# Performance work log

Hardware: AMD Instinct MI355X
Metric: run time of the kernel (lower is better)

The kernel has to match this reference:

```python
import jax, jax.numpy as jnp
import numpy as np

DIM = 512
MAX_STEP = 4
SLOTS = 8


def _lin(x, w, b):
    # torch nn.Linear convention: w is [out, in]
    return jnp.matmul(x, jnp.swapaxes(w, -1, -2)) + b


def setup_inputs() -> dict:
    B, L, HW, d, S, K = 512, 32, 196, DIM, MAX_STEP, SLOTS
    ks = iter(jax.random.split(jax.random.key(0), 48))
    def rn(shape, scale=1.0):
        return scale * jax.random.normal(next(ks), shape, dtype=jnp.float32)
    p = 0.05  # weight init scale
    z = lambda *s: jnp.zeros(s, jnp.float32)
    return {
        'context': rn((B, L, d)),
        'question': rn((B, 2 * d)),
        'knowledge': rn((B, d, HW)),
        'kb_proj': rn((B, d, HW)),
        'control': rn((B, d)),
        'memory': rn((B, d)),
        'history': rn((B, d, K)),
        'Wt_sequential': jnp.zeros((B, 1, K), jnp.float32).at[:, :, 0].set(1.0),
        # ControlUnit params (per-step position-aware linears, control-question linear, attention linear)
        'ctrl_pos_w': rn((S, d, 2 * d), p), 'ctrl_pos_b': z(S, d),
        'ctrl_cq_w': rn((d, 2 * d), p), 'ctrl_cq_b': z(d),
        'ctrl_attn_w': rn((1, d), p), 'ctrl_attn_b': z(1),
        # ReadUnit params (memory proj, concat proj, attention)
        'read_mem_w': rn((d, d), p), 'read_mem_b': z(d),
        'read_cat_w': rn((d, 2 * d), p), 'read_cat_b': z(d),
        'read_attn_w': rn((1, d), p), 'read_attn_b': z(1),
        # ReadMemory params (same structure, over the slot history)
        'rm_mem_w': rn((d, d), p), 'rm_mem_b': z(d),
        'rm_cat_w': rn((d, 2 * d), p), 'rm_cat_b': z(d),
        'rm_attn_w': rn((1, d), p), 'rm_attn_b': z(1),
        # WriteUnit (no self-attention / no memory gate)
        'write_w': rn((d, 2 * d), p), 'write_b': z(d),
        # linear_read gate MLP (2d -> 2d -> 1)
        'lr_w1': rn((2 * d, 2 * d), p), 'lr_b1': z(2 * d),
        'lr_w2': rn((1, 2 * d), p), 'lr_b2': z(1),
        # linear_read_history gate MLP
        'lrh_w1': rn((2 * d, 2 * d), p), 'lrh_b1': z(2 * d),
        'lrh_w2': rn((1, 2 * d), p), 'lrh_b2': z(1),
        # linear_layer_mix_context MLP (d -> d -> 3)
        'mix_w1': rn((d, d), p), 'mix_b1': z(d),
        'mix_w2': rn((3, d), p), 'mix_b2': z(3),
    }


def _forward(context, question, knowledge, kb_proj, control, memory, history, Wt_sequential,
             ctrl_pos_w, ctrl_pos_b, ctrl_cq_w, ctrl_cq_b, ctrl_attn_w, ctrl_attn_b,
             read_mem_w, read_mem_b, read_cat_w, read_cat_b, read_attn_w, read_attn_b,
             rm_mem_w, rm_mem_b, rm_cat_w, rm_cat_b, rm_attn_w, rm_attn_b,
             write_w, write_b, lr_w1, lr_b1, lr_w2, lr_b2,
             lrh_w1, lrh_b1, lrh_w2, lrh_b2, mix_w1, mix_b1, mix_w2, mix_b2):
    K = history.shape[2]
    # shift-by-one circulant matrix, matches the hard-coded convolution_kernel for slots in {4,6,8}
    conv_kernel = jnp.roll(jnp.eye(K, dtype=history.dtype), -1, axis=1)
    for i in range(MAX_STEP):
        # --- ControlUnit: attention over contextual words ---
        pa = _lin(question, ctrl_pos_w[i], ctrl_pos_b[i])                                  # [B,d]
        cqi = _lin(jnp.concatenate([control, pa], axis=1), ctrl_cq_w, ctrl_cq_b)           # [B,d]
        cvi = jax.nn.softmax(_lin(cqi[:, None, :] * context, ctrl_attn_w, ctrl_attn_b), axis=1)  # [B,L,1]
        control = jnp.sum(cvi * context, axis=1)                                           # [B,d]
        # --- ReadUnit: attention over the knowledge base ---
        mem_p = _lin(memory, read_mem_w, read_mem_b)[:, :, None]                           # [B,d,1]
        cat = jnp.concatenate([mem_p * kb_proj, kb_proj], axis=1)                          # [B,2d,HW]
        feat = _lin(cat.transpose(0, 2, 1), read_cat_w, read_cat_b)                        # [B,HW,d]
        attn = jax.nn.softmax(_lin(feat * control[:, None, :], read_attn_w, read_attn_b), axis=1)
        attn = attn.transpose(0, 2, 1)                                                     # [B,1,HW]
        read = jnp.sum(attn * knowledge, axis=2)                                           # [B,d]
        # --- ReadMemory: attention over the slot history ---
        memh = _lin(memory, rm_mem_w, rm_mem_b)[:, :, None]                                # [B,d,1]
        cath = jnp.concatenate([memh * history, history], axis=1)                          # [B,2d,K]
        feath = _lin(cath.transpose(0, 2, 1), rm_cat_w, rm_cat_b)                          # [B,K,d]
        rvi_h = jax.nn.softmax(_lin(feath * control[:, None, :], rm_attn_w, rm_attn_b), axis=1).transpose(0, 2, 1)  # [B,1,K]
        read_h = jnp.sum(rvi_h * history, axis=2)                                          # [B,d]
        # --- gates ---
        gkb = jax.nn.sigmoid(_lin(jax.nn.elu(_lin(jnp.concatenate([control, read], axis=1), lr_w1, lr_b1)), lr_w2, lr_b2))      # [B,1]
        gmem = jax.nn.sigmoid(_lin(jax.nn.elu(_lin(jnp.concatenate([control, read_h], axis=1), lrh_w1, lrh_b1)), lrh_w2, lrh_b2))  # [B,1]
        # --- gated addressable memory write (NTM-style) ---
        wts = Wt_sequential[:, 0, :]                                                       # [B,K]
        W = (gmem * rvi_h[:, 0, :] + wts * (1.0 - gmem)) * gkb                             # [B,K]
        history = history * (1.0 - W[:, None, :]) + read[:, :, None] * W[:, None, :]       # erase + add
        first = (1.0 - gmem) * gkb                                                         # [B,1]
        Wt_sequential = ((wts @ conv_kernel) * first + wts * (1.0 - first))[:, None, :]    # [B,1,K]
        # --- context mixing + write ---
        now_ctx = gkb * read
        last_ctx = gmem * read_h
        latest_ctx = (1.0 - gkb) * last_ctx + now_ctx
        cwv = jax.nn.softmax(_lin(jax.nn.elu(_lin(control, mix_w1, mix_b1)), mix_w2, mix_b2), axis=1)  # [B,3]
        ctx_read = cwv[:, 0:1] * now_ctx + cwv[:, 1:2] * last_ctx + cwv[:, 2:3] * latest_ctx
        memory = _lin(jnp.concatenate([ctx_read, memory], axis=1), write_w, write_b)       # [B,d]
    return memory


reference = _forward
```

## Files before the change

kernel.cpp:

```cpp
#include <hip/hip_runtime.h>
#include <cstddef>

constexpr int NB   = 512;
constexpr int ND   = 512;
constexpr int NL   = 32;
constexpr int NHW  = 196;
constexpr int NK   = 8;
constexpr int NSTEP = 4;

typedef __attribute__((ext_vector_type(8))) short short8v;
typedef __attribute__((ext_vector_type(4))) float f32x4;

__device__ __forceinline__ void splitbf(float x, short& h, short& l) {
    unsigned u  = __float_as_uint(x);
    unsigned hb = (u + 0x7FFFu + ((u >> 16) & 1u)) & 0xFFFF0000u;
    h = (short)(hb >> 16);
    float rem = x - __uint_as_float(hb);
    unsigned v = __float_as_uint(rem);
    l = (short)((v + 0x7FFFu + ((v >> 16) & 1u)) >> 16);
}
__device__ __forceinline__ unsigned short f2bf(float x) {
    unsigned u = __float_as_uint(x);
    return (unsigned short)((u + 0x7FFFu + ((u >> 16) & 1u)) >> 16);
}
__device__ __forceinline__ float bf2f(unsigned short h) {
    return __uint_as_float(((unsigned)h) << 16);
}

struct GP {
    const short *A1h, *A1l, *A2h, *A2l;
    const short *Bh, *Bl;
    const float* bias;
    float* C; short* Ch; short* Cl;
    int lda1, lda2, k1, N, K, ntN, tile0;
};
struct GPG { GP p[3]; int np; };

template<int ACT>
__global__ __launch_bounds__(256) void ggemm_k(GPG g)
{
    __shared__ short Ah[32][40], Al[32][40], Bh_s[64][40], Bl_s[64][40];
    const int flat = blockIdx.x;
    int pi = 0;
    if (g.np > 1 && flat >= g.p[1].tile0) pi = 1;
    if (g.np > 2 && flat >= g.p[2].tile0) pi = 2;
    const GP p = g.p[pi];
    const int local = flat - p.tile0;
    const int my = local / p.ntN, nx = local - my * p.ntN;
    const int m0 = my * 32, n0 = nx * 64;
    const int t = threadIdx.x, lane = t & 63, wid = t >> 6;
    const int wr = wid >> 1, wc = wid & 1;
    const int lr = lane & 15, lk = (lane >> 4) * 8;
    const int ar = (t & 127) >> 2, ak = (t & 3) * 8;
    const bool alo = t >= 128;
    const int br = t >> 2, bk = (t & 3) * 8;

    f32x4 acc0 = {}, acc1 = {};
    for (int kt = 0; kt < p.K; kt += 32) {
        {
            const int gk = kt + ak;
            const short* srcp = (gk < p.k1)
                ? (alo ? p.A1l : p.A1h) + (size_t)(m0 + ar) * p.lda1 + gk
                : (alo ? p.A2l : p.A2h) + (size_t)(m0 + ar) * p.lda2 + (gk - p.k1);
            short8v v = *(const short8v*)srcp;
            if (alo) *(short8v*)&Al[ar][ak] = v;
            else     *(short8v*)&Ah[ar][ak] = v;
        }
        {
            const size_t off = (size_t)(n0 + br) * p.K + kt + bk;
            *(short8v*)&Bh_s[br][bk] = *(const short8v*)(p.Bh + off);
            *(short8v*)&Bl_s[br][bk] = *(const short8v*)(p.Bl + off);
        }
        __syncthreads();
        short8v ah  = *(short8v*)&Ah[wr * 16 + lr][lk];
        short8v al  = *(short8v*)&Al[wr * 16 + lr][lk];
        short8v bh0 = *(short8v*)&Bh_s[wc * 32      + lr][lk];
        short8v bh1 = *(short8v*)&Bh_s[wc * 32 + 16 + lr][lk];
        short8v bl0 = *(short8v*)&Bl_s[wc * 32      + lr][lk];
        short8v bl1 = *(short8v*)&Bl_s[wc * 32 + 16 + lr][lk];
        acc0 = __builtin_amdgcn_mfma_f32_16x16x32_bf16(ah, bh0, acc0, 0, 0, 0);
        acc1 = __builtin_amdgcn_mfma_f32_16x16x32_bf16(ah, bh1, acc1, 0, 0, 0);
        acc0 = __builtin_amdgcn_mfma_f32_16x16x32_bf16(al, bh0, acc0, 0, 0, 0);
        acc1 = __builtin_amdgcn_mfma_f32_16x16x32_bf16(al, bh1, acc1, 0, 0, 0);
        acc0 = __builtin_amdgcn_mfma_f32_16x16x32_bf16(ah, bl0, acc0, 0, 0, 0);
        acc1 = __builtin_amdgcn_mfma_f32_16x16x32_bf16(ah, bl1, acc1, 0, 0, 0);
        __syncthreads();
    }
    const int r0 = m0 + wr * 16 + ((lane >> 4) << 2);
    const int cb = n0 + wc * 32 + lr;
    #pragma unroll
    for (int fc = 0; fc < 2; ++fc) {
        const f32x4& a = fc ? acc1 : acc0;
        const int col = cb + fc * 16;
        const float badd = p.bias ? p.bias[col] : 0.f;
        #pragma unroll
        for (int rr = 0; rr < 4; ++rr) {
            float x = a[rr] + badd;
            if (ACT == 1) x = (x > 0.f) ? x : (expf(x) - 1.f);
            const size_t idx = (size_t)(r0 + rr) * p.N + col;
            if (p.C) p.C[idx] = x;
            if (p.Ch) { short h, l; splitbf(x, h, l); p.Ch[idx] = h; p.Cl[idx] = l; }
        }
    }
}

struct WSeg { const float* src; short* dh; short* dl; int n; };
struct WTab { WSeg s[12]; int total; };

__global__ __launch_bounds__(256) void wconv_k(WTab tab)
{
    int i = blockIdx.x * 256 + threadIdx.x;
    if (i >= tab.total) return;
    int seg = 0, off = i;
    while (off >= tab.s[seg].n) { off -= tab.s[seg].n; ++seg; }
    short h, l; splitbf(tab.s[seg].src[off], h, l);
    tab.s[seg].dh[off] = h;
    tab.s[seg].dl[off] = l;
}

__global__ __launch_bounds__(256) void tconv_k(
    const float* s0, short* dh0, short* dl0,
    const float* s1, short* dh1, short* dl1)
{
    const float* src = blockIdx.z ? s1 : s0;
    short* dh = blockIdx.z ? dh1 : dh0;
    short* dl = blockIdx.z ? dl1 : dl0;
    __shared__ float tile[32][33];
    const int n0 = blockIdx.x * 32, k0 = blockIdx.y * 32;
    const int tx = threadIdx.x & 31, ty = threadIdx.x >> 5;
    for (int i = ty; i < 32; i += 8)
        tile[i][tx] = src[(size_t)(k0 + i) * 1024 + n0 + tx];
    __syncthreads();
    for (int i = ty; i < 32; i += 8) {
        short h, l; splitbf(tile[tx][i], h, l);
        dh[(size_t)(n0 + i) * 512 + k0 + tx] = h;
        dl[(size_t)(n0 + i) * 512 + k0 + tx] = l;
    }
}

__global__ __launch_bounds__(512) void ctrl_attn_k(
    const float* __restrict__ cqi, const float* __restrict__ context,
    const float* __restrict__ attn_w, const float* __restrict__ read_attn_w,
    const float* __restrict__ rm_attn_w,
    short* __restrict__ ct_h, short* __restrict__ ct_l,
    short* __restrict__ cw_h, short* __restrict__ cw_l,
    short* __restrict__ cx_h, short* __restrict__ cx_l)
{
    const int b = blockIdx.x, t = threadIdx.x;
    const int lane = t & 63, w = t >> 6;
    __shared__ float q[ND];
    __shared__ float p[NL];
    const float* ctx = context + (size_t)b * NL * ND;

    q[t] = cqi[(size_t)b * ND + t] * attn_w[t];
    __syncthreads();

    for (int l = w; l < NL; l += 8) {
        float s = 0.f;
        const float* row = ctx + (size_t)l * ND;
        #pragma unroll
        for (int d = lane; d < ND; d += 64) s += q[d] * row[d];
        #pragma unroll
        for (int o = 32; o; o >>= 1) s += __shfl_down(s, o);
        if (lane == 0) p[l] = s;
    }
    __syncthreads();
    if (t == 0) {
        float mx = p[0];
        for (int l = 1; l < NL; ++l) mx = fmaxf(mx, p[l]);
        float sum = 0.f;
        for (int l = 0; l < NL; ++l) { float e = expf(p[l] - mx); p[l] = e; sum += e; }
        const float inv = 1.f / sum;
        for (int l = 0; l < NL; ++l) p[l] *= inv;
    }
    __syncthreads();
    float a = 0.f;
    #pragma unroll 8
    for (int l = 0; l < NL; ++l) a += p[l] * ctx[(size_t)l * ND + t];
    const size_t ix = (size_t)b * ND + t;
    short h, l2;
    splitbf(a, h, l2);                     ct_h[ix] = h; ct_l[ix] = l2;
    splitbf(a * read_attn_w[t], h, l2);    cw_h[ix] = h; cw_l[ix] = l2;
    splitbf(a * rm_attn_w[t],  h, l2);     cx_h[ix] = h; cx_l[ix] = l2;
}

template<int FIRST>
__global__ __launch_bounds__(256) void kbsh_k(
    const float* __restrict__ kbp_f32, unsigned short* __restrict__ kbp_bf,
    const float* __restrict__ mpc, const float* __restrict__ u,
    float* __restrict__ s_part,
    const float* __restrict__ hist, const float* __restrict__ uh,
    float* __restrict__ rvi, float* __restrict__ read_h,
    short* __restrict__ rh_h, short* __restrict__ rh_l)
{
    __shared__ float sh[NK * ND + ND];
    __shared__ float sred[NK], pk[NK];
    const int bx = blockIdx.x, t = threadIdx.x;
    const int lane = t & 63, w = t >> 6;

    if (bx < 4 * NB) {
        const int jc = bx >> 9, b = bx & 511;
        float* v = sh;
        const int j0 = jc * 128;
        if (t < 128) {
            const int j = j0 + t;
            v[t] = mpc[(size_t)b * 1024 + j] * u[(size_t)b * 1024 + j]
                 + u[(size_t)b * 1024 + 512 + j];
        }
        __syncthreads();
        if (t < NHW) {
            const size_t base = (size_t)b * ND * NHW + (size_t)j0 * NHW + t;
            float s = 0.f;
            #pragma unroll 4
            for (int j = 0; j < 128; ++j) {
                float x;
                if (FIRST) {
                    x = kbp_f32[base + (size_t)j * NHW];
                    kbp_bf[base + (size_t)j * NHW] = f2bf(x);
                } else {
                    x = bf2f(kbp_bf[base + (size_t)j * NHW]);
                }
                s += x * v[j];
            }
            s_part[((size_t)jc * NB + b) * 200 + t] = s;
        }
    } else {
        const int b = bx - 4 * NB;
        float* ht = sh;
        float* vh = sh + NK * ND;
        const float* hb = hist + (size_t)b * ND * NK;

        for (int dd = t; dd < ND; dd += 256) {
            float4 h0 = *(const float4*)&hb[(size_t)dd * NK];
            float4 h1 = *(const float4*)&hb[(size_t)dd * NK + 4];
            ht[0 * ND + dd] = h0.x; ht[1 * ND + dd] = h0.y;
            ht[2 * ND + dd] = h0.z; ht[3 * ND + dd] = h0.w;
            ht[4 * ND + dd] = h1.x; ht[5 * ND + dd] = h1.y;
            ht[6 * ND + dd] = h1.z; ht[7 * ND + dd] = h1.w;
            vh[dd] = mpc[(size_t)b * 1024 + 512 + dd] * uh[(size_t)b * 1024 + dd]
                   + uh[(size_t)b * 1024 + 512 + dd];
        }
        __syncthreads();

        for (int k = w; k < NK; k += 4) {
            float s = 0.f;
            #pragma unroll 4
            for (int dd = lane; dd < ND; dd += 64) s += ht[k * ND + dd] * vh[dd];
            #pragma unroll
            for (int o = 32; o; o >>= 1) s += __shfl_down(s, o);
            if (lane == 0) sred[k] = s;
        }
        __syncthreads();
        if (t == 0) {
            float mx = sred[0];
            #pragma unroll
            for (int k = 1; k < NK; ++k) mx = fmaxf(mx, sred[k]);
            float ev[NK]; float sum = 0.f;
            #pragma unroll
            for (int k = 0; k < NK; ++k) { ev[k] = expf(sred[k] - mx); sum += ev[k]; }
            const float inv = 1.f / sum;
            #pragma unroll
            for (int k = 0; k < NK; ++k) { float pv = ev[k] * inv; pk[k] = pv; rvi[(size_t)b * NK + k] = pv; }
        }
        __syncthreads();
        for (int dd = t; dd < ND; dd += 256) {
            float a = 0.f;
// ... 166 lines not shown
{
    (void)in_sizes; (void)n_in; (void)out_size; (void)ws_size;
    const float* context    = (const float*)d_in[0];
    const float* question   = (const float*)d_in[1];
    const float* knowledge  = (const float*)d_in[2];
    const float* kb_proj    = (const float*)d_in[3];
    const float* control0   = (const float*)d_in[4];
    const float* memory0    = (const float*)d_in[5];
    const float* history0   = (const float*)d_in[6];
    const float* wt0        = (const float*)d_in[7];
    const float* ctrl_pos_w = (const float*)d_in[8];
    const float* ctrl_pos_b = (const float*)d_in[9];
    const float* ctrl_cq_w  = (const float*)d_in[10];
    const float* ctrl_cq_b  = (const float*)d_in[11];
    const float* ctrl_attn_w= (const float*)d_in[12];
    const float* read_mem_w = (const float*)d_in[14];
    const float* read_mem_b = (const float*)d_in[15];
    const float* read_cat_w = (const float*)d_in[16];
    const float* read_attn_w= (const float*)d_in[18];
    const float* rm_mem_w   = (const float*)d_in[20];
    const float* rm_mem_b   = (const float*)d_in[21];
    const float* rm_cat_w   = (const float*)d_in[22];
    const float* rm_attn_w  = (const float*)d_in[24];
    const float* write_w    = (const float*)d_in[26];
    const float* write_b    = (const float*)d_in[27];
    const float* lr_w1      = (const float*)d_in[28];
    const float* lr_b1      = (const float*)d_in[29];
    const float* lr_w2      = (const float*)d_in[30];
    const float* lr_b2      = (const float*)d_in[31];
    const float* lrh_w1     = (const float*)d_in[32];
    const float* lrh_b1     = (const float*)d_in[33];
    const float* lrh_w2     = (const float*)d_in[34];
    const float* lrh_b2     = (const float*)d_in[35];
    const float* mix_w1     = (const float*)d_in[36];
    const float* mix_b1     = (const float*)d_in[37];
    const float* mix_w2     = (const float*)d_in[38];
    const float* mix_b2     = (const float*)d_in[39];

    float* f = (float*)d_ws;
    auto takef = [&](size_t n) { float* p = f; f += n; return p; };
    float* cqi    = takef((size_t)NB * ND);
    float* mpc    = takef((size_t)NB * 1024);
    float* u      = takef((size_t)NB * 1024);
    float* uh     = takef((size_t)NB * 1024);
    float* readv  = takef((size_t)NB * ND);
    float* read_h = takef((size_t)NB * ND);
    float* rvi    = takef((size_t)NB * NK);
    float* g1a    = takef((size_t)NB * 1024);
    float* g1b    = takef((size_t)NB * 1024);
    float* m1buf  = takef((size_t)NB * ND);
    float* hist   = takef((size_t)NB * ND * NK);
    float* wts    = takef((size_t)NB * NK);
    float* s_part = takef((size_t)4 * NB * 200);
    float* bcat   = takef(1024);

    uintptr_t fa = ((uintptr_t)f + 15) & ~(uintptr_t)15;
    short* s = (short*)fa;
    auto takes = [&](size_t n) { short* p = s; s += n; return p; };
    short* cpw_h = takes((size_t)2048 * 1024); short* cpw_l = takes((size_t)2048 * 1024);
    short* cqw_h = takes((size_t)512 * 1024);  short* cqw_l = takes((size_t)512 * 1024);
    short* wmc_h = takes((size_t)1024 * 512);  short* wmc_l = takes((size_t)1024 * 512);
    short* rcw_h = takes((size_t)1024 * 512);  short* rcw_l = takes((size_t)1024 * 512);
    short* rmw_h = takes((size_t)1024 * 512);  short* rmw_l = takes((size_t)1024 * 512);
    short* lrw_h = takes((size_t)1024 * 1024); short* lrw_l = takes((size_t)1024 * 1024);
    short* lhw_h = takes((size_t)1024 * 1024); short* lhw_l = takes((size_t)1024 * 1024);
    short* mxw_h = takes((size_t)512 * 512);   short* mxw_l = takes((size_t)512 * 512);
    short* ww_h  = takes((size_t)512 * 1024);  short* ww_l  = takes((size_t)512 * 1024);
    short* q_h   = takes((size_t)512 * 1024);  short* q_l   = takes((size_t)512 * 1024);
    short* c0_h  = takes((size_t)NB * ND);     short* c0_l  = takes((size_t)NB * ND);
    short* m0_h  = takes((size_t)NB * ND);     short* m0_l  = takes((size_t)NB * ND);
    short* pa_h  = takes((size_t)NB * 2048);   short* pa_l  = takes((size_t)NB * 2048);
    short* ct_h  = takes((size_t)NB * ND);     short* ct_l  = takes((size_t)NB * ND);
    short* cw_h  = takes((size_t)NB * ND);     short* cw_l  = takes((size_t)NB * ND);
    short* cwh_h = takes((size_t)NB * ND);     short* cwh_l = takes((size_t)NB * ND);
    short* rv_h  = takes((size_t)NB * ND);     short* rv_l  = takes((size_t)NB * ND);
    short* rh_h  = takes((size_t)NB * ND);     short* rh_l  = takes((size_t)NB * ND);
    short* cx_h  = takes((size_t)NB * ND);     short* cx_l  = takes((size_t)NB * ND);
    short* mA_h  = takes((size_t)NB * ND);     short* mA_l  = takes((size_t)NB * ND);
    short* mB_h  = takes((size_t)NB * ND);     short* mB_l  = takes((size_t)NB * ND);
    short* mC_h  = takes((size_t)NB * ND);     short* mC_l  = takes((size_t)NB * ND);
    unsigned short* kbp_bf = (unsigned short*)s;
    unsigned short* knw_bf = kbp_bf + (size_t)NB * ND * NHW;

    hipMemcpyAsync(hist, history0, sizeof(float) * NB * ND * NK, hipMemcpyDeviceToDevice, stream);
    hipMemcpyAsync(wts,  wt0,      sizeof(float) * NB * NK,      hipMemcpyDeviceToDevice, stream);
    hipMemcpyAsync(bcat,       read_mem_b, sizeof(float) * 512, hipMemcpyDeviceToDevice, stream);
    hipMemcpyAsync(bcat + 512, rm_mem_b,   sizeof(float) * 512, hipMemcpyDeviceToDevice, stream);

    WTab tab;
    tab.s[0]  = {ctrl_pos_w, cpw_h, cpw_l, 2048 * 1024};
    tab.s[1]  = {ctrl_cq_w,  cqw_h, cqw_l, 512 * 1024};
    tab.s[2]  = {read_mem_w, wmc_h, wmc_l, 512 * 512};
    tab.s[3]  = {rm_mem_w,   wmc_h + 512 * 512, wmc_l + 512 * 512, 512 * 512};
    tab.s[4]  = {lr_w1,  lrw_h, lrw_l, 1024 * 1024};
    tab.s[5]  = {lrh_w1, lhw_h, lhw_l, 1024 * 1024};
    tab.s[6]  = {mix_w1, mxw_h, mxw_l, 512 * 512};
    tab.s[7]  = {write_w, ww_h, ww_l, 512 * 1024};
    tab.s[8]  = {question, q_h, q_l, 512 * 1024};
    tab.s[9]  = {control0, c0_h, c0_l, 512 * 512};
    tab.s[10] = {memory0,  m0_h, m0_l, 512 * 512};
    tab.s[11] = {nullptr, nullptr, nullptr, 0};
    tab.total = 2048*1024 + 512*1024 + 512*512 + 512*512 + 1024*1024 + 1024*1024
              + 512*512 + 512*1024 + 512*1024 + 512*512 + 512*512;
    wconv_k<<<dim3((tab.total + 255) / 256), dim3(256), 0, stream>>>(tab);
    tconv_k<<<dim3(32, 16, 2), dim3(256), 0, stream>>>(read_cat_w, rcw_h, rcw_l,
                                                       rm_cat_w,  rmw_h, rmw_l);

    auto P = [](const short* A1h, const short* A1l, int lda1, int k1,
                const short* A2h, const short* A2l, int lda2,
                const short* Bh, const short* Bl, const float* bias,
                float* C, short* Ch, short* Cl, int N, int K, int tile0) {
        GP q; q.A1h = A1h; q.A1l = A1l; q.A2h = A2h; q.A2l = A2l;
        q.Bh = Bh; q.Bl = Bl; q.bias = bias; q.C = C; q.Ch = Ch; q.Cl = Cl;
        q.lda1 = lda1; q.lda2 = lda2; q.k1 = k1; q.N = N; q.K = K;
        q.ntN = N / 64; q.tile0 = tile0;
        return q;
    };
    auto tilesOf = [](int N) { return (NB / 32) * (N / 64); };
    auto GG = [&](GPG g, int total, int act) {
        if (act) ggemm_k<1><<<dim3(total), dim3(256), 0, stream>>>(g);
        else     ggemm_k<0><<<dim3(total), dim3(256), 0, stream>>>(g);
    };

    {
        GPG g; g.np = 1;
        g.p[0] = P(q_h, q_l, 1024, 1024, q_h, q_l, 1024, cpw_h, cpw_l, ctrl_pos_b,
                   nullptr, pa_h, pa_l, 2048, 1024, 0);
        GG(g, tilesOf(2048), 0);
    }

    const short* mems_h[4] = {m0_h, mA_h, mB_h, mC_h};
    const short* mems_l[4] = {m0_l, mA_l, mB_l, mC_l};
    const short* ctl_h = c0_h;
    const short* ctl_l = c0_l;

    for (int i = 0; i < NSTEP; ++i) {
        {
            GPG g; int nt = 0, np = 0;
            if (i > 0) {
                g.p[np++] = P(cx_h, cx_l, ND, ND, mems_h[i - 1], mems_l[i - 1], ND,
                              ww_h, ww_l, write_b, nullptr,
                              (short*)mems_h[i], (short*)mems_l[i], ND, 1024, nt);
                nt += tilesOf(ND);
            }
            g.p[np++] = P(ctl_h, ctl_l, ND, ND, pa_h + (size_t)i * ND, pa_l + (size_t)i * ND, 2048,
                          cqw_h, cqw_l, ctrl_cq_b, cqi, nullptr, nullptr, ND, 1024, nt);
            nt += tilesOf(ND);
            g.np = np;
            GG(g, nt, 0);
        }
        ctrl_attn_k<<<dim3(NB), dim3(512), 0, stream>>>(cqi, context, ctrl_attn_w,
                                                        read_attn_w, rm_attn_w,
                                                        ct_h, ct_l, cw_h, cw_l, cwh_h, cwh_l);
        ctl_h = ct_h; ctl_l = ct_l;
        {
            GPG g; g.np = 3;
            g.p[0] = P(mems_h[i], mems_l[i], ND, ND, mems_h[i], mems_l[i], ND,
                       wmc_h, wmc_l, bcat, mpc, nullptr, nullptr, 1024, 512, 0);
            g.p[1] = P(cw_h, cw_l, ND, ND, cw_h, cw_l, ND,
                       rcw_h, rcw_l, nullptr, u, nullptr, nullptr, 1024, 512, 256);
            g.p[2] = P(cwh_h, cwh_l, ND, ND, cwh_h, cwh_l, ND,
                       rmw_h, rmw_l, nullptr, uh, nullptr, nullptr, 1024, 512, 512);
            GG(g, 768, 0);
        }
        if (i == 0)
            kbsh_k<1><<<dim3(5 * NB), dim3(256), 0, stream>>>(kb_proj, kbp_bf, mpc, u, s_part,
                                                              hist, uh, rvi, read_h, rh_h, rh_l);
        else
            kbsh_k<0><<<dim3(5 * NB), dim3(256), 0, stream>>>(kb_proj, kbp_bf, mpc, u, s_part,
                                                              hist, uh, rvi, read_h, rh_h, rh_l);
        if (i == 0)
            kb_read_k<1><<<dim3(8, NB), dim3(256), 0, stream>>>(knowledge, knw_bf, s_part,
                                                                readv, rv_h, rv_l);
        else
            kb_read_k<0><<<dim3(8, NB), dim3(256), 0, stream>>>(knowledge, knw_bf, s_part,
                                                                readv, rv_h, rv_l);
        {
            GPG g; g.np = 3;
            g.p[0] = P(ct_h, ct_l, ND, ND, rv_h, rv_l, ND,
                       lrw_h, lrw_l, lr_b1, g1a, nullptr, nullptr, 1024, 1024, 0);
            g.p[1] = P(ct_h, ct_l, ND, ND, rh_h, rh_l, ND,
                       lhw_h, lhw_l, lrh_b1, g1b, nullptr, nullptr, 1024, 1024, 256);
            g.p[2] = P(ct_h, ct_l, ND, ND, ct_h, ct_l, ND,
                       mxw_h, mxw_l, mix_b1, m1buf, nullptr, nullptr, 512, 512, 512);
            GG(g, 640, 1);
        }
        update2_k<<<dim3(NB), dim3(256), 0, stream>>>(g1a, g1b, m1buf,
                                                      lr_w2, lr_b2, lrh_w2, lrh_b2,
                                                      mix_w2, mix_b2, rvi, readv, read_h,
                                                      hist, wts, cx_h, cx_l);
    }
    {
        GPG g; g.np = 1;
        g.p[0] = P(cx_h, cx_l, ND, ND, mems_h[3], mems_l[3], ND,
                   ww_h, ww_l, write_b, (float*)d_out, nullptr, nullptr, ND, 1024, 0);
        GG(g, tilesOf(ND), 0);
    }
}
```

Before: 960.2 us.

## Regroup per-step GEMMs into fused launches and double GEMM K-tile

Reschedules the per-step work. The memory-projection GEMM now runs as extra blocks inside the control-attention kernel, the next step's control-question GEMM is folded into the gate-GEMM launch, and the mix GEMM moves to the read-projection launch. The activation choice becomes a runtime per-problem flag so different activations can share one launch. The GEMM K tile also grows from 32 to 64 to halve the number of sync iterations. The intent is fewer launches and more concurrent blocks per launch, at the cost of more shared memory per block (about 27 KB), which may lower occupancy, plus a runtime branch in the epilogue.

```diff
diff --git a/kernel.cpp b/kernel.cpp
--- a/kernel.cpp
+++ b/kernel.cpp
@@ -28,62 +28,71 @@
 }
 
 struct GP {
-    const short *A1h, *A1l, *A2h, *A2l;
-    const short *Bh, *Bl;
+    const short *A1h, *A1l, *A2h, *A2l, *Bh, *Bl;
     const float* bias;
     float* C; short* Ch; short* Cl;
-    int lda1, lda2, k1, N, K, ntN, tile0;
+    int lda1, lda2, k1, N, K, ntN, t0, act;
 };
 struct GPG { GP p[3]; int np; };
 
-template<int ACT>
-__global__ __launch_bounds__(256) void ggemm_k(GPG g)
-{
-    __shared__ short Ah[32][40], Al[32][40], Bh_s[64][40], Bl_s[64][40];
-    const int flat = blockIdx.x;
-    int pi = 0;
-    if (g.np > 1 && flat >= g.p[1].tile0) pi = 1;
-    if (g.np > 2 && flat >= g.p[2].tile0) pi = 2;
-    const GP p = g.p[pi];
-    const int local = flat - p.tile0;
+#define SMEM_GEMM 27648
+
+__device__ void dev_gemm(const GP& p, int local, int t, char* smem)
+{
+    short (*Ah)[72] = (short(*)[72])(smem);
+    short (*Al)[72] = (short(*)[72])(smem + 4608);
+    short (*Bh)[72] = (short(*)[72])(smem + 9216);
+    short (*Bl)[72] = (short(*)[72])(smem + 18432);
     const int my = local / p.ntN, nx = local - my * p.ntN;
     const int m0 = my * 32, n0 = nx * 64;
-    const int t = threadIdx.x, lane = t & 63, wid = t >> 6;
+    const int lane = t & 63, wid = t >> 6;
     const int wr = wid >> 1, wc = wid & 1;
     const int lr = lane & 15, lk = (lane >> 4) * 8;
-    const int ar = (t & 127) >> 2, ak = (t & 3) * 8;
+    const int ac = t & 127;
     const bool alo = t >= 128;
-    const int br = t >> 2, bk = (t & 3) * 8;
 
     f32x4 acc0 = {}, acc1 = {};
-    for (int kt = 0; kt < p.K; kt += 32) {
-        {
-            const int gk = kt + ak;
+    for (int kt = 0; kt < p.K; kt += 64) {
+        #pragma unroll
+        for (int cc = 0; cc < 2; ++cc) {
+            const int c = ac + cc * 128;
+            const int r = c >> 3, kc = (c & 7) * 8;
+            const int gk = kt + kc;
             const short* srcp = (gk < p.k1)
-                ? (alo ? p.A1l : p.A1h) + (size_t)(m0 + ar) * p.lda1 + gk
-                : (alo ? p.A2l : p.A2h) + (size_t)(m0 + ar) * p.lda2 + (gk - p.k1);
+                ? (alo ? p.A1l : p.A1h) + (size_t)(m0 + r) * p.lda1 + gk
+                : (alo ? p.A2l : p.A2h) + (size_t)(m0 + r) * p.lda2 + (gk - p.k1);
             short8v v = *(const short8v*)srcp;
-            if (alo) *(short8v*)&Al[ar][ak] = v;
-            else     *(short8v*)&Ah[ar][ak] = v;
-        }
-        {
-            const size_t off = (size_t)(n0 + br) * p.K + kt + bk;
-            *(short8v*)&Bh_s[br][bk] = *(const short8v*)(p.Bh + off);
-            *(short8v*)&Bl_s[br][bk] = *(const short8v*)(p.Bl + off);
+            if (alo) *(short8v*)&Al[r][kc] = v;
+            else     *(short8v*)&Ah[r][kc] = v;
+        }
+        #pragma unroll
+        for (int cc = 0; cc < 2; ++cc) {
+            const int c = t + cc * 256;
+            const int r = c >> 3, kc = (c & 7) * 8;
+            const size_t off = (size_t)(n0 + r) * p.K + kt + kc;
+            *(short8v*)&Bh[r][kc] = *(const short8v*)(p.Bh + off);
+            *(short8v*)&Bl[r][kc] = *(const short8v*)(p.Bl + off);
         }
         __syncthreads();
-        short8v ah  = *(short8v*)&Ah[wr * 16 + lr][lk];
-        short8v al  = *(short8v*)&Al[wr * 16 + lr][lk];
-        short8v bh0 = *(short8v*)&Bh_s[wc * 32      + lr][lk];
-        short8v bh1 = *(short8v*)&Bh_s[wc * 32 + 16 + lr][lk];
-        short8v bl0 = *(short8v*)&Bl_s[wc * 32      + lr][lk];
-        short8v bl1 = *(short8v*)&Bl_s[wc * 32 + 16 + lr][lk];
-        acc0 = __builtin_amdgcn_mfma_f32_16x16x32_bf16(ah, bh0, acc0, 0, 0, 0);
-        acc1 = __builtin_amdgcn_mfma_f32_16x16x32_bf16(ah, bh1, acc1, 0, 0, 0);
-        acc0 = __builtin_amdgcn_mfma_f32_16x16x32_bf16(al, bh0, acc0, 0, 0, 0);
-        acc1 = __builtin_amdgcn_mfma_f32_16x16x32_bf16(al, bh1, acc1, 0, 0, 0);
-        acc0 = __builtin_amdgcn_mfma_f32_16x16x32_bf16(ah, bl0, acc0, 0, 0, 0);
-        acc1 = __builtin_amdgcn_mfma_f32_16x16x32_bf16(ah, bl1, acc1, 0, 0, 0);
+        const int arow = wr * 16 + lr, br0 = wc * 32 + lr, br1 = br0 + 16;
+        short8v ah0 = *(short8v*)&Ah[arow][lk], ah1 = *(short8v*)&Ah[arow][lk + 32];
+        short8v al0 = *(short8v*)&Al[arow][lk], al1 = *(short8v*)&Al[arow][lk + 32];
+        short8v bh00 = *(short8v*)&Bh[br0][lk], bh01 = *(short8v*)&Bh[br0][lk + 32];
+        short8v bh10 = *(short8v*)&Bh[br1][lk], bh11 = *(short8v*)&Bh[br1][lk + 32];
+        short8v bl00 = *(short8v*)&Bl[br0][lk], bl01 = *(short8v*)&Bl[br0][lk + 32];
+        short8v bl10 = *(short8v*)&Bl[br1][lk], bl11 = *(short8v*)&Bl[br1][lk + 32];
+        acc0 = __builtin_amdgcn_mfma_f32_16x16x32_bf16(ah0, bh00, acc0, 0, 0, 0);
+        acc1 = __builtin_amdgcn_mfma_f32_16x16x32_bf16(ah0, bh10, acc1, 0, 0, 0);
+        acc0 = __builtin_amdgcn_mfma_f32_16x16x32_bf16(al0, bh00, acc0, 0, 0, 0);
+        acc1 = __builtin_amdgcn_mfma_f32_16x16x32_bf16(al0, bh10, acc1, 0, 0, 0);
+        acc0 = __builtin_amdgcn_mfma_f32_16x16x32_bf16(ah0, bl00, acc0, 0, 0, 0);
+        acc1 = __builtin_amdgcn_mfma_f32_16x16x32_bf16(ah0, bl10, acc1, 0, 0, 0);
+        acc0 = __builtin_amdgcn_mfma_f32_16x16x32_bf16(ah1, bh01, acc0, 0, 0, 0);
+        acc1 = __builtin_amdgcn_mfma_f32_16x16x32_bf16(ah1, bh11, acc1, 0, 0, 0);
+        acc0 = __builtin_amdgcn_mfma_f32_16x16x32_bf16(al1, bh01, acc0, 0, 0, 0);
+        acc1 = __builtin_amdgcn_mfma_f32_16x16x32_bf16(al1, bh11, acc1, 0, 0, 0);
+        acc0 = __builtin_amdgcn_mfma_f32_16x16x32_bf16(ah1, bl01, acc0, 0, 0, 0);
+        acc1 = __builtin_amdgcn_mfma_f32_16x16x32_bf16(ah1, bl11, acc1, 0, 0, 0);
         __syncthreads();
     }
     const int r0 = m0 + wr * 16 + ((lane >> 4) << 2);
@@ -96,12 +105,26 @@
         #pragma unroll
         for (int rr = 0; rr < 4; ++rr) {
             float x = a[rr] + badd;
-            if (ACT == 1) x = (x > 0.f) ? x : (expf(x) - 1.f);
+            if (p.act == 1) x = (x > 0.f) ? x : (expf(x) - 1.f);
             const size_t idx = (size_t)(r0 + rr) * p.N + col;
             if (p.C) p.C[idx] = x;
             if (p.Ch) { short h, l; splitbf(x, h, l); p.Ch[idx] = h; p.Cl[idx] = l; }
         }
     }
+}
+
+__device__ __forceinline__ void run_gemms(const GPG& g, int bid, int tid, char* smem)
+{
+    int pi = 0;
+    if (g.np > 1 && bid >= g.p[1].t0) pi = 1;
+    if (g.np > 2 && bid >= g.p[2].t0) pi = 2;
+    dev_gemm(g.p[pi], bid - g.p[pi].t0, tid, smem);
+}
+
+__global__ __launch_bounds__(256) void ggemm_k(GPG g)
+{
+    __shared__ __align__(16) char smem[SMEM_GEMM];
+    run_gemms(g, blockIdx.x, threadIdx.x, smem);
 }
 
 struct WSeg { const float* src; short* dh; short* dl; int n; };
@@ -138,24 +161,29 @@
     }
 }
 
-__global__ __launch_bounds__(512) void ctrl_attn_k(
+__global__ __launch_bounds__(256) void ctrlmpc_k(
     const float* __restrict__ cqi, const float* __restrict__ context,
     const float* __restrict__ attn_w, const float* __restrict__ read_attn_w,
     const float* __restrict__ rm_attn_w,
     short* __restrict__ ct_h, short* __restrict__ ct_l,
     short* __restrict__ cw_h, short* __restrict__ cw_l,
-    short* __restrict__ cx_h, short* __restrict__ cx_l)
-{
-    const int b = blockIdx.x, t = threadIdx.x;
-    const int lane = t & 63, w = t >> 6;
-    __shared__ float q[ND];
-    __shared__ float p[NL];
+    short* __restrict__ cx_h, short* __restrict__ cx_l,
+    GPG g)
+{
+    __shared__ __align__(16) char smem[SMEM_GEMM];
+    const int bid = blockIdx.x, tid = threadIdx.x;
+    if (bid >= NB) {
+        run_gemms(g, bid - NB, tid, smem);
+        return;
+    }
+    float* q = (float*)smem;
+    float* p = q + ND;
+    const int b = bid, lane = tid & 63, w = tid >> 6;
     const float* ctx = context + (size_t)b * NL * ND;
 
-    q[t] = cqi[(size_t)b * ND + t] * attn_w[t];
-    __syncthreads();
-
-    for (int l = w; l < NL; l += 8) {
+    for (int d = tid; d < ND; d += 256) q[d] = cqi[(size_t)b * ND + d] * attn_w[d];
+    __syncthreads();
+    for (int l = w; l < NL; l += 4) {
         float s = 0.f;
         const float* row = ctx + (size_t)l * ND;
         #pragma unroll
@@ -165,7 +193,7 @@
         if (lane == 0) p[l] = s;
     }
     __syncthreads();
-    if (t == 0) {
+    if (tid == 0) {
         float mx = p[0];
         for (int l = 1; l < NL; ++l) mx = fmaxf(mx, p[l]);
         float sum = 0.f;
@@ -174,14 +202,16 @@
         for (int l = 0; l < NL; ++l) p[l] *= inv;
     }
     __syncthreads();
-    float a = 0.f;
-    #pragma unroll 8
-    for (int l = 0; l < NL; ++l) a += p[l] * ctx[(size_t)l * ND + t];
-    const size_t ix = (size_t)b * ND + t;
-    short h, l2;
-    splitbf(a, h, l2);                     ct_h[ix] = h; ct_l[ix] = l2;
-    splitbf(a * read_attn_w[t], h, l2);    cw_h[ix] = h; cw_l[ix] = l2;
-    splitbf(a * rm_attn_w[t],  h, l2);     cx_h[ix] = h; cx_l[ix] = l2;
+    for (int d = tid; d < ND; d += 256) {
+        float a = 0.f;
+        #pragma unroll 8
+        for (int l = 0; l < NL; ++l) a += p[l] * ctx[(size_t)l * ND + d];
+        const size_t ix = (size_t)b * ND + d;
+        short h, l2;
+        splitbf(a, h, l2);                     ct_h[ix] = h; ct_l[ix] = l2;
+        splitbf(a * read_attn_w[d], h, l2);    cw_h[ix] = h; cw_l[ix] = l2;
+        splitbf(a * rm_attn_w[d],  h, l2);     cx_h[ix] = h; cx_l[ix] = l2;
+    }
 }
 
 template<int FIRST>
@@ -541,59 +571,59 @@
     auto P = [](const short* A1h, const short* A1l, int lda1, int k1,
                 const short* A2h, const short* A2l, int lda2,
                 const short* Bh, const short* Bl, const float* bias,
-                float* C, short* Ch, short* Cl, int N, int K, int tile0) {
+                float* C, short* Ch, short* Cl, int N, int K, int t0, int act) {
         GP q; q.A1h = A1h; q.A1l = A1l; q.A2h = A2h; q.A2l = A2l;
         q.Bh = Bh; q.Bl = Bl; q.bias = bias; q.C = C; q.Ch = Ch; q.Cl = Cl;
         q.lda1 = lda1; q.lda2 = lda2; q.k1 = k1; q.N = N; q.K = K;
-        q.ntN = N / 64; q.tile0 = tile0;
+        q.ntN = N / 64; q.t0 = t0; q.act = act;
         return q;
     };
     auto tilesOf = [](int N) { return (NB / 32) * (N / 64); };
-    auto GG = [&](GPG g, int total, int act) {
-        if (act) ggemm_k<1><<<dim3(total), dim3(256), 0, stream>>>(g);
-        else     ggemm_k<0><<<dim3(total), dim3(256), 0, stream>>>(g);
+    auto GG = [&](GPG g, int total) {
+        ggemm_k<<<dim3(total), dim3(256), 0, stream>>>(g);
     };
 
     {
         GPG g; g.np = 1;
         g.p[0] = P(q_h, q_l, 1024, 1024, q_h, q_l, 1024, cpw_h, cpw_l, ctrl_pos_b,
-                   nullptr, pa_h, pa_l, 2048, 1024, 0);
-        GG(g, tilesOf(2048), 0);
+                   nullptr, pa_h, pa_l, 2048, 1024, 0, 0);
+        GG(g, tilesOf(2048));
+    }
+    {
+        GPG g; g.np = 1;
+        g.p[0] = P(c0_h, c0_l, ND, ND, pa_h, pa_l, 2048,
+                   cqw_h, cqw_l, ctrl_cq_b, cqi, nullptr, nullptr, ND, 1024, 0, 0);
+        GG(g, tilesOf(ND));
     }
 
     const short* mems_h[4] = {m0_h, mA_h, mB_h, mC_h};
     const short* mems_l[4] = {m0_l, mA_l, mB_l, mC_l};
-    const short* ctl_h = c0_h;
-    const short* ctl_l = c0_l;
 
     for (int i = 0; i < NSTEP; ++i) {
+        if (i > 0) {
+            GPG g; g.np = 1;
+            g.p[0] = P(cx_h, cx_l, ND, ND, mems_h[i - 1], mems_l[i - 1], ND,
+                       ww_h, ww_l, write_b, nullptr,
+                       (short*)mems_h[i], (short*)mems_l[i], ND, 1024, 0, 0);
+            GG(g, tilesOf(ND));
+        }
         {
-            GPG g; int nt = 0, np = 0;
-            if (i > 0) {
-                g.p[np++] = P(cx_h, cx_l, ND, ND, mems_h[i - 1], mems_l[i - 1], ND,
-                              ww_h, ww_l, write_b, nullptr,
-                              (short*)mems_h[i], (short*)mems_l[i], ND, 1024, nt);
-                nt += tilesOf(ND);
-            }
-            g.p[np++] = P(ctl_h, ctl_l, ND, ND, pa_h + (size_t)i * ND, pa_l + (size_t)i * ND, 2048,
-                          cqw_h, cqw_l, ctrl_cq_b, cqi, nullptr, nullptr, ND, 1024, nt);
-            nt += tilesOf(ND);
-            g.np = np;
-            GG(g, nt, 0);
-        }
-        ctrl_attn_k<<<dim3(NB), dim3(512), 0, stream>>>(cqi, context, ctrl_attn_w,
-                                                        read_attn_w, rm_attn_w,
-                                                        ct_h, ct_l, cw_h, cw_l, cwh_h, cwh_l);
-        ctl_h = ct_h; ctl_l = ct_l;
+            GPG g; g.np = 1;
+            g.p[0] = P(mems_h[i], mems_l[i], ND, ND, mems_h[i], mems_l[i], ND,
+                       wmc_h, wmc_l, bcat, mpc, nullptr, nullptr, 1024, 512, 0, 0);
+            ctrlmpc_k<<<dim3(NB + tilesOf(1024)), dim3(256), 0, stream>>>(
+                cqi, context, ctrl_attn_w, read_attn_w, rm_attn_w,
+                ct_h, ct_l, cw_h, cw_l, cwh_h, cwh_l, g);
+        }
         {
             GPG g; g.np = 3;
-            g.p[0] = P(mems_h[i], mems_l[i], ND, ND, mems_h[i], mems_l[i], ND,
-                       wmc_h, wmc_l, bcat, mpc, nullptr, nullptr, 1024, 512, 0);
-            g.p[1] = P(cw_h, cw_l, ND, ND, cw_h, cw_l, ND,
-                       rcw_h, rcw_l, nullptr, u, nullptr, nullptr, 1024, 512, 256);
-            g.p[2] = P(cwh_h, cwh_l, ND, ND, cwh_h, cwh_l, ND,
-                       rmw_h, rmw_l, nullptr, uh, nullptr, nullptr, 1024, 512, 512);
-            GG(g, 768, 0);
+            g.p[0] = P(cw_h, cw_l, ND, ND, cw_h, cw_l, ND,
+                       rcw_h, rcw_l, nullptr, u, nullptr, nullptr, 1024, 512, 0, 0);
+            g.p[1] = P(cwh_h, cwh_l, ND, ND, cwh_h, cwh_l, ND,
+                       rmw_h, rmw_l, nullptr, uh, nullptr, nullptr, 1024, 512, 256, 0);
+            g.p[2] = P(ct_h, ct_l, ND, ND, ct_h, ct_l, ND,
+                       mxw_h, mxw_l, mix_b1, m1buf, nullptr, nullptr, 512, 512, 512, 1);
+            GG(g, 640);
         }
         if (i == 0)
             kbsh_k<1><<<dim3(5 * NB), dim3(256), 0, stream>>>(kb_proj, kbp_bf, mpc, u, s_part,
@@ -608,14 +638,19 @@
             kb_read_k<0><<<dim3(8, NB), dim3(256), 0, stream>>>(knowledge, knw_bf, s_part,
                                                                 readv, rv_h, rv_l);
         {
-            GPG g; g.np = 3;
+            GPG g; g.np = (i < NSTEP - 1) ? 3 : 2;
             g.p[0] = P(ct_h, ct_l, ND, ND, rv_h, rv_l, ND,
-                       lrw_h, lrw_l, lr_b1, g1a, nullptr, nullptr, 1024, 1024, 0);
+                       lrw_h, lrw_l, lr_b1, g1a, nullptr, nullptr, 1024, 1024, 0, 1);
             g.p[1] = P(ct_h, ct_l, ND, ND, rh_h, rh_l, ND,
-                       lhw_h, lhw_l, lrh_b1, g1b, nullptr, nullptr, 1024, 1024, 256);
-            g.p[2] = P(ct_h, ct_l, ND, ND, ct_h, ct_l, ND,
-                       mxw_h, mxw_l, mix_b1, m1buf, nullptr, nullptr, 512, 512, 512);
-            GG(g, 640, 1);
+                       lhw_h, lhw_l, lrh_b1, g1b, nullptr, nullptr, 1024, 1024, 256, 1);
+            int nt = 512;
+            if (i < NSTEP - 1) {
+                g.p[2] = P(ct_h, ct_l, ND, ND,
+                           pa_h + (size_t)(i + 1) * ND, pa_l + (size_t)(i + 1) * ND, 2048,
+                           cqw_h, cqw_l, ctrl_cq_b, cqi, nullptr, nullptr, ND, 1024, 512, 0);
+                nt += tilesOf(ND);
+            }
+            GG(g, nt);
         }
         update2_k<<<dim3(NB), dim3(256), 0, stream>>>(g1a, g1b, m1buf,
                                                       lr_w2, lr_b2, lrh_w2, lrh_b2,
@@ -625,7 +660,7 @@
     {
         GPG g; g.np = 1;
         g.p[0] = P(cx_h, cx_l, ND, ND, mems_h[3], mems_l[3], ND,
-                   ww_h, ww_l, write_b, (float*)d_out, nullptr, nullptr, ND, 1024, 0);
-        GG(g, tilesOf(ND), 0);
-    }
-}
+                   ww_h, ww_l, write_b, (float*)d_out, nullptr, nullptr, ND, 1024, 0, 0);
+        GG(g, tilesOf(ND));
+    }
+}
```

Result: slower. 1.046 ms (+8.9%).

## Merge prologue copies and conversions into one kernel, split position GEMM

Applied to the files above, without the earlier changes.

Folds the four device-to-device memcpys, the weight bf16 split conversion and the transposed conversion into a single prolog kernel, so fewer launches are issued. The position-aware projection GEMM is split: the step-0 slice runs first, and the step-0 control-question GEMM is co-launched with the remaining position slices. The GEMM kernel takes activation as a runtime flag and gains an explicit output stride. This trades a few launches and serial dependencies for runtime branching inside the GEMM.

```diff
diff --git a/kernel.cpp b/kernel.cpp
--- a/kernel.cpp
+++ b/kernel.cpp
@@ -28,27 +28,22 @@
 }
 
 struct GP {
-    const short *A1h, *A1l, *A2h, *A2l;
-    const short *Bh, *Bl;
+    const short *A1h, *A1l, *A2h, *A2l, *Bh, *Bl;
     const float* bias;
     float* C; short* Ch; short* Cl;
-    int lda1, lda2, k1, N, K, ntN, tile0;
+    int lda1, lda2, k1, N, K, ntN, t0, act, ldc;
 };
 struct GPG { GP p[3]; int np; };
 
-template<int ACT>
-__global__ __launch_bounds__(256) void ggemm_k(GPG g)
-{
-    __shared__ short Ah[32][40], Al[32][40], Bh_s[64][40], Bl_s[64][40];
-    const int flat = blockIdx.x;
-    int pi = 0;
-    if (g.np > 1 && flat >= g.p[1].tile0) pi = 1;
-    if (g.np > 2 && flat >= g.p[2].tile0) pi = 2;
-    const GP p = g.p[pi];
-    const int local = flat - p.tile0;
+__device__ void dev_gemm(const GP& p, int local, int t, char* smem)
+{
+    short (*Ah)[40]   = (short(*)[40])(smem);
+    short (*Al)[40]   = (short(*)[40])(smem + 2560);
+    short (*Bh_s)[40] = (short(*)[40])(smem + 5120);
+    short (*Bl_s)[40] = (short(*)[40])(smem + 10240);
     const int my = local / p.ntN, nx = local - my * p.ntN;
     const int m0 = my * 32, n0 = nx * 64;
-    const int t = threadIdx.x, lane = t & 63, wid = t >> 6;
+    const int lane = t & 63, wid = t >> 6;
     const int wr = wid >> 1, wc = wid & 1;
     const int lr = lane & 15, lk = (lane >> 4) * 8;
     const int ar = (t & 127) >> 2, ak = (t & 3) * 8;
@@ -96,45 +91,60 @@
         #pragma unroll
         for (int rr = 0; rr < 4; ++rr) {
             float x = a[rr] + badd;
-            if (ACT == 1) x = (x > 0.f) ? x : (expf(x) - 1.f);
-            const size_t idx = (size_t)(r0 + rr) * p.N + col;
+            if (p.act == 1) x = (x > 0.f) ? x : (expf(x) - 1.f);
+            const size_t idx = (size_t)(r0 + rr) * p.ldc + col;
             if (p.C) p.C[idx] = x;
             if (p.Ch) { short h, l; splitbf(x, h, l); p.Ch[idx] = h; p.Cl[idx] = l; }
         }
     }
 }
 
+__global__ __launch_bounds__(256) void ggemm_k(GPG g)
+{
+    __shared__ __align__(16) char smem[15360];
+    const int bid = blockIdx.x;
+    int pi = 0;
+    if (g.np > 1 && bid >= g.p[1].t0) pi = 1;
+    if (g.np > 2 && bid >= g.p[2].t0) pi = 2;
+    dev_gemm(g.p[pi], bid - g.p[pi].t0, threadIdx.x, smem);
+}
+
 struct WSeg { const float* src; short* dh; short* dl; int n; };
-struct WTab { WSeg s[12]; int total; };
-
-__global__ __launch_bounds__(256) void wconv_k(WTab tab)
-{
-    int i = blockIdx.x * 256 + threadIdx.x;
-    if (i >= tab.total) return;
-    int seg = 0, off = i;
-    while (off >= tab.s[seg].n) { off -= tab.s[seg].n; ++seg; }
-    short h, l; splitbf(tab.s[seg].src[off], h, l);
-    tab.s[seg].dh[off] = h;
-    tab.s[seg].dl[off] = l;
-}
-
-__global__ __launch_bounds__(256) void tconv_k(
-    const float* s0, short* dh0, short* dl0,
-    const float* s1, short* dh1, short* dl1)
-{
-    const float* src = blockIdx.z ? s1 : s0;
-    short* dh = blockIdx.z ? dh1 : dh0;
-    short* dl = blockIdx.z ? dl1 : dl0;
+struct Prolog {
+    WSeg s[15];
+    int total, nconvblk;
+    const float* t0src; short* t0h; short* t0l;
+    const float* t1src; short* t1h; short* t1l;
+};
+
+__global__ __launch_bounds__(256) void prolog_k(Prolog pb)
+{
     __shared__ float tile[32][33];
-    const int n0 = blockIdx.x * 32, k0 = blockIdx.y * 32;
-    const int tx = threadIdx.x & 31, ty = threadIdx.x >> 5;
-    for (int i = ty; i < 32; i += 8)
-        tile[i][tx] = src[(size_t)(k0 + i) * 1024 + n0 + tx];
-    __syncthreads();
-    for (int i = ty; i < 32; i += 8) {
-        short h, l; splitbf(tile[tx][i], h, l);
-        dh[(size_t)(n0 + i) * 512 + k0 + tx] = h;
-        dl[(size_t)(n0 + i) * 512 + k0 + tx] = l;
+    const int bid = blockIdx.x, tid = threadIdx.x;
+    if (bid < pb.nconvblk) {
+        int i = bid * 256 + tid;
+        if (i >= pb.total) return;
+        int seg = 0, off = i;
+        while (off >= pb.s[seg].n) { off -= pb.s[seg].n; ++seg; }
+        const WSeg sg = pb.s[seg];
+        if (sg.dl) { short h, l; splitbf(sg.src[off], h, l); sg.dh[off] = h; sg.dl[off] = l; }
+        else       { ((float*)sg.dh)[off] = sg.src[off]; }
+    } else {
+        const int tb = bid - pb.nconvblk;
+        const float* src = (tb >= 512) ? pb.t1src : pb.t0src;
+        short* dh = (tb >= 512) ? pb.t1h : pb.t0h;
+        short* dl = (tb >= 512) ? pb.t1l : pb.t0l;
+        const int rem = tb & 511;
+        const int n0 = (rem & 31) * 32, k0 = (rem >> 5) * 32;
+        const int tx = tid & 31, ty = tid >> 5;
+        for (int i = ty; i < 32; i += 8)
+            tile[i][tx] = src[(size_t)(k0 + i) * 1024 + n0 + tx];
+        __syncthreads();
+        for (int i = ty; i < 32; i += 8) {
+            short h, l; splitbf(tile[tx][i], h, l);
+            dh[(size_t)(n0 + i) * 512 + k0 + tx] = h;
+            dl[(size_t)(n0 + i) * 512 + k0 + tx] = l;
+        }
     }
 }
 
@@ -514,86 +524,88 @@
     unsigned short* kbp_bf = (unsigned short*)s;
     unsigned short* knw_bf = kbp_bf + (size_t)NB * ND * NHW;
 
-    hipMemcpyAsync(hist, history0, sizeof(float) * NB * ND * NK, hipMemcpyDeviceToDevice, stream);
-    hipMemcpyAsync(wts,  wt0,      sizeof(float) * NB * NK,      hipMemcpyDeviceToDevice, stream);
-    hipMemcpyAsync(bcat,       read_mem_b, sizeof(float) * 512, hipMemcpyDeviceToDevice, stream);
-    hipMemcpyAsync(bcat + 512, rm_mem_b,   sizeof(float) * 512, hipMemcpyDeviceToDevice, stream);
-
-    WTab tab;
-    tab.s[0]  = {ctrl_pos_w, cpw_h, cpw_l, 2048 * 1024};
-    tab.s[1]  = {ctrl_cq_w,  cqw_h, cqw_l, 512 * 1024};
-    tab.s[2]  = {read_mem_w, wmc_h, wmc_l, 512 * 512};
-    tab.s[3]  = {rm_mem_w,   wmc_h + 512 * 512, wmc_l + 512 * 512, 512 * 512};
-    tab.s[4]  = {lr_w1,  lrw_h, lrw_l, 1024 * 1024};
-    tab.s[5]  = {lrh_w1, lhw_h, lhw_l, 1024 * 1024};
-    tab.s[6]  = {mix_w1, mxw_h, mxw_l, 512 * 512};
-    tab.s[7]  = {write_w, ww_h, ww_l, 512 * 1024};
-    tab.s[8]  = {question, q_h, q_l, 512 * 1024};
-    tab.s[9]  = {control0, c0_h, c0_l, 512 * 512};
-    tab.s[10] = {memory0,  m0_h, m0_l, 512 * 512};
-    tab.s[11] = {nullptr, nullptr, nullptr, 0};
-    tab.total = 2048*1024 + 512*1024 + 512*512 + 512*512 + 1024*1024 + 1024*1024
-              + 512*512 + 512*1024 + 512*1024 + 512*512 + 512*512;
-    wconv_k<<<dim3((tab.total + 255) / 256), dim3(256), 0, stream>>>(tab);
-    tconv_k<<<dim3(32, 16, 2), dim3(256), 0, stream>>>(read_cat_w, rcw_h, rcw_l,
-                                                       rm_cat_w,  rmw_h, rmw_l);
+    Prolog pb;
+    pb.s[0]  = {ctrl_pos_w, cpw_h, cpw_l, 2048 * 1024};
+    pb.s[1]  = {ctrl_cq_w,  cqw_h, cqw_l, 512 * 1024};
+    pb.s[2]  = {read_mem_w, wmc_h, wmc_l, 512 * 512};
+    pb.s[3]  = {rm_mem_w,   wmc_h + 512 * 512, wmc_l + 512 * 512, 512 * 512};
+    pb.s[4]  = {lr_w1,  lrw_h, lrw_l, 1024 * 1024};
+    pb.s[5]  = {lrh_w1, lhw_h, lhw_l, 1024 * 1024};
+    pb.s[6]  = {mix_w1, mxw_h, mxw_l, 512 * 512};
+    pb.s[7]  = {write_w, ww_h, ww_l, 512 * 1024};
+    pb.s[8]  = {question, q_h, q_l, 512 * 1024};
+    pb.s[9]  = {control0, c0_h, c0_l, 512 * 512};
+    pb.s[10] = {memory0,  m0_h, m0_l, 512 * 512};
+    pb.s[11] = {history0, (short*)hist, nullptr, NB * ND * NK};
+    pb.s[12] = {wt0,      (short*)wts,  nullptr, NB * NK};
+    pb.s[13] = {read_mem_b, (short*)bcat, nullptr, 512};
+    pb.s[14] = {rm_mem_b, (short*)(bcat + 512), nullptr, 512};
+    pb.total = 2048*1024 + 512*1024 + 512*512 + 512*512 + 1024*1024 + 1024*1024
+             + 512*512 + 512*1024 + 512*1024 + 512*512 + 512*512
+             + NB*ND*NK + NB*NK + 1024;
+    pb.nconvblk = (pb.total + 255) / 256;
+    pb.t0src = read_cat_w; pb.t0h = rcw_h; pb.t0l = rcw_l;
+    pb.t1src = rm_cat_w;   pb.t1h = rmw_h; pb.t1l = rmw_l;
+    prolog_k<<<dim3(pb.nconvblk + 1024), dim3(256), 0, stream>>>(pb);
 
     auto P = [](const short* A1h, const short* A1l, int lda1, int k1,
                 const short* A2h, const short* A2l, int lda2,
                 const short* Bh, const short* Bl, const float* bias,
-                float* C, short* Ch, short* Cl, int N, int K, int tile0) {
+                float* C, short* Ch, short* Cl, int N, int K, int t0, int act, int ldc) {
         GP q; q.A1h = A1h; q.A1l = A1l; q.A2h = A2h; q.A2l = A2l;
         q.Bh = Bh; q.Bl = Bl; q.bias = bias; q.C = C; q.Ch = Ch; q.Cl = Cl;
         q.lda1 = lda1; q.lda2 = lda2; q.k1 = k1; q.N = N; q.K = K;
-        q.ntN = N / 64; q.tile0 = tile0;
+        q.ntN = N / 64; q.t0 = t0; q.act = act; q.ldc = ldc;
         return q;
     };
     auto tilesOf = [](int N) { return (NB / 32) * (N / 64); };
-    auto GG = [&](GPG g, int total, int act) {
-        if (act) ggemm_k<1><<<dim3(total), dim3(256), 0, stream>>>(g);
-        else     ggemm_k<0><<<dim3(total), dim3(256), 0, stream>>>(g);
+    auto GG = [&](GPG g, int total) {
+        ggemm_k<<<dim3(total), dim3(256), 0, stream>>>(g);
     };
 
     {
         GPG g; g.np = 1;
         g.p[0] = P(q_h, q_l, 1024, 1024, q_h, q_l, 1024, cpw_h, cpw_l, ctrl_pos_b,
-                   nullptr, pa_h, pa_l, 2048, 1024, 0);
-        GG(g, tilesOf(2048), 0);
+                   nullptr, pa_h, pa_l, 512, 1024, 0, 0, 2048);
+        GG(g, 128);
+    }
+    {
+        GPG g; g.np = 2;
+        g.p[0] = P(c0_h, c0_l, ND, ND, pa_h, pa_l, 2048,
+                   cqw_h, cqw_l, ctrl_cq_b, cqi, nullptr, nullptr, ND, 1024, 0, 0, ND);
+        g.p[1] = P(q_h, q_l, 1024, 1024, q_h, q_l, 1024,
+                   cpw_h + (size_t)512 * 1024, cpw_l + (size_t)512 * 1024,
+                   ctrl_pos_b + 512, nullptr, pa_h + 512, pa_l + 512,
+                   1536, 1024, 128, 0, 2048);
+        GG(g, 128 + 384);
     }
 
     const short* mems_h[4] = {m0_h, mA_h, mB_h, mC_h};
     const short* mems_l[4] = {m0_l, mA_l, mB_l, mC_l};
-    const short* ctl_h = c0_h;
-    const short* ctl_l = c0_l;
 
     for (int i = 0; i < NSTEP; ++i) {
-        {
-            GPG g; int nt = 0, np = 0;
-            if (i > 0) {
-                g.p[np++] = P(cx_h, cx_l, ND, ND, mems_h[i - 1], mems_l[i - 1], ND,
-                              ww_h, ww_l, write_b, nullptr,
-                              (short*)mems_h[i], (short*)mems_l[i], ND, 1024, nt);
-                nt += tilesOf(ND);
-            }
-            g.p[np++] = P(ctl_h, ctl_l, ND, ND, pa_h + (size_t)i * ND, pa_l + (size_t)i * ND, 2048,
-                          cqw_h, cqw_l, ctrl_cq_b, cqi, nullptr, nullptr, ND, 1024, nt);
-            nt += tilesOf(ND);
-            g.np = np;
-            GG(g, nt, 0);
+        if (i > 0) {
+            GPG g; g.np = 2;
+            g.p[0] = P(cx_h, cx_l, ND, ND, mems_h[i - 1], mems_l[i - 1], ND,
+                       ww_h, ww_l, write_b, nullptr,
+                       (short*)mems_h[i], (short*)mems_l[i], ND, 1024, 0, 0, ND);
+            g.p[1] = P(ct_h, ct_l, ND, ND, pa_h + (size_t)i * ND, pa_l + (size_t)i * ND, 2048,
+                       cqw_h, cqw_l, ctrl_cq_b, cqi, nullptr, nullptr, ND, 1024,
+                       tilesOf(ND), 0, ND);
+            GG(g, 2 * tilesOf(ND));
         }
         ctrl_attn_k<<<dim3(NB), dim3(512), 0, stream>>>(cqi, context, ctrl_attn_w,
                                                         read_attn_w, rm_attn_w,
                                                         ct_h, ct_l, cw_h, cw_l, cwh_h, cwh_l);
-        ctl_h = ct_h; ctl_l = ct_l;
         {
             GPG g; g.np = 3;
             g.p[0] = P(mems_h[i], mems_l[i], ND, ND, mems_h[i], mems_l[i], ND,
-                       wmc_h, wmc_l, bcat, mpc, nullptr, nullptr, 1024, 512, 0);
+                       wmc_h, wmc_l, bcat, mpc, nullptr, nullptr, 1024, 512, 0, 0, 1024);
             g.p[1] = P(cw_h, cw_l, ND, ND, cw_h, cw_l, ND,
-                       rcw_h, rcw_l, nullptr, u, nullptr, nullptr, 1024, 512, 256);
+                       rcw_h, rcw_l, nullptr, u, nullptr, nullptr, 1024, 512, 256, 0, 1024);
             g.p[2] = P(cwh_h, cwh_l, ND, ND, cwh_h, cwh_l, ND,
-                       rmw_h, rmw_l, nullptr, uh, nullptr, nullptr, 1024, 512, 512);
-            GG(g, 768, 0);
+                       rmw_h, rmw_l, nullptr, uh, nullptr, nullptr, 1024, 512, 512, 0, 1024);
+            GG(g, 768);
         }
         if (i == 0)
             kbsh_k<1><<<dim3(5 * NB), dim3(256), 0, stream>>>(kb_proj, kbp_bf, mpc, u, s_part,
@@ -610,12 +622,12 @@
         {
             GPG g; g.np = 3;
             g.p[0] = P(ct_h, ct_l, ND, ND, rv_h, rv_l, ND,
-                       lrw_h, lrw_l, lr_b1, g1a, nullptr, nullptr, 1024, 1024, 0);
+                       lrw_h, lrw_l, lr_b1, g1a, nullptr, nullptr, 1024, 1024, 0, 1, 1024);
             g.p[1] = P(ct_h, ct_l, ND, ND, rh_h, rh_l, ND,
-                       lhw_h, lhw_l, lrh_b1, g1b, nullptr, nullptr, 1024, 1024, 256);
+                       lhw_h, lhw_l, lrh_b1, g1b, nullptr, nullptr, 1024, 1024, 256, 1, 1024);
             g.p[2] = P(ct_h, ct_l, ND, ND, ct_h, ct_l, ND,
-                       mxw_h, mxw_l, mix_b1, m1buf, nullptr, nullptr, 512, 512, 512);
-            GG(g, 640, 1);
+                       mxw_h, mxw_l, mix_b1, m1buf, nullptr, nullptr, 512, 512, 512, 1, 512);
+            GG(g, 640);
         }
         update2_k<<<dim3(NB), dim3(256), 0, stream>>>(g1a, g1b, m1buf,
                                                       lr_w2, lr_b2, lrh_w2, lrh_b2,
@@ -625,7 +637,7 @@
     {
         GPG g; g.np = 1;
         g.p[0] = P(cx_h, cx_l, ND, ND, mems_h[3], mems_l[3], ND,
-                   ww_h, ww_l, write_b, (float*)d_out, nullptr, nullptr, ND, 1024, 0);
-        GG(g, tilesOf(ND), 0);
-    }
-}
+                   ww_h, ww_l, write_b, (float*)d_out, nullptr, nullptr, ND, 1024, 0, 0, ND);
+        GG(g, tilesOf(ND));
+    }
+}
```

New measurement: 1.010 ms. 5.2% more time.
